# Kernel optimization log

Measured on AMD Instinct MI355X. Metric: run time of the kernel, lower is better.

Reference implementation:

```python
import jax, jax.numpy as jnp
import numpy as np

EPS = 1e-4


def setup_inputs() -> dict:
    key = jax.random.key(0)
    ks = jax.random.split(key, 16)
    N, D, H, K = 262144, 162, 256, 30
    s = 0.05  # weight init scale
    return {
        "Yh": jax.random.uniform(ks[0], (N, D), dtype=jnp.float32),
        "u": jax.random.uniform(ks[1], (1,), dtype=jnp.float32),
        "W1": jax.random.normal(ks[2], (D, H), dtype=jnp.float32) * s,
        "b1": jnp.zeros((H,), jnp.float32),
        "W2": jax.random.normal(ks[3], (H, H), dtype=jnp.float32) * s,
        "b2": jnp.zeros((H,), jnp.float32),
        "Wa": jax.random.normal(ks[4], (H, K), dtype=jnp.float32) * s,
        "ba": jnp.zeros((K,), jnp.float32),
        "Wb": jax.random.normal(ks[5], (H, K), dtype=jnp.float32) * s,
        "bb": jnp.zeros((K,), jnp.float32),
        "Wd1": jax.random.normal(ks[6], (K, H), dtype=jnp.float32) * s,
        "bd1": jnp.zeros((H,), jnp.float32),
        "Wd2": jax.random.normal(ks[7], (H, D), dtype=jnp.float32) * s,
        "bd2": jnp.zeros((D,), jnp.float32),
    }


def _stick_segments(v):
    # pi_k = v_k * prod_{j<k} (1 - v_j)  (vectorized exclusive cumprod,
    # replacing the original per-dim Python loop)
    cp = jnp.cumprod(1.0 - v, axis=1)  # [N, K]
    excl = jnp.concatenate([jnp.ones_like(v[:, :1]), cp[:, :-1]], axis=1)
    return v * excl


def reference(Yh, u, W1, b1, W2, b2, Wa, ba, Wb, bb, Wd1, bd1, Wd2, bd2):
    # encode_hsi: dense MLP -> positive Kumaraswamy params (softplus heads)
    h = jax.nn.relu(Yh @ W1 + b1)
    h = jax.nn.relu(h @ W2 + b2)
    alpha = jax.nn.softplus(h @ Wa + ba) + EPS  # param1_hsi [N, K]
    beta = jax.nn.softplus(h @ Wb + bb) + EPS   # param2_hsi [N, K]
    # Kumaraswamy reparametrization with a single shared uniform sample
    uu = u[0] * 0.98 + 0.01  # Uniform(0.01, 0.99) scalar
    v = (1.0 - uu ** (1.0 / beta)) ** (1.0 / alpha)  # [N, K]
    # set_v_K_to_one: force last stick proportion to 1
    v = jnp.concatenate([v[:, :-1], jnp.ones_like(v[:, :1])], axis=1)
    pi_h = _stick_segments(v)  # [N, K], rows sum to 1
    # decode: MLP -> sigmoid (positive outputs, recon.log() finite)
    d = jax.nn.relu(pi_h @ Wd1 + bd1)
    recon = jax.nn.sigmoid(d @ Wd2 + bd2)  # [N, D]
    return recon, alpha, beta, pi_h
```

## Files before the change

### kernel.cpp

```cpp
#include <hip/hip_runtime.h>
#include <hip/hip_bf16.h>

#define N_ROWS 262144
#define D_IN 162
#define K_DIM 30
#define ROWS 32

using bf16_t = __hip_bfloat16;
typedef __attribute__((ext_vector_type(8))) short bf16x8;
typedef __attribute__((ext_vector_type(4))) float f32x4;

__device__ __forceinline__ int swz_byte(int row, int col) {
  int b = (row << 9) + (col << 1);
  return b ^ ((row & 7) << 4);
}

__device__ __forceinline__ uint32_t bf16b(float x) {
  return (uint32_t)__builtin_bit_cast(unsigned short, __float2bfloat16(x));
}
__device__ __forceinline__ uint32_t pack2(float lo, float hi) {
  return bf16b(lo) | (bf16b(hi) << 16);
}
__device__ __forceinline__ float unpk_lo(uint32_t p) {
  return __bfloat162float(__builtin_bit_cast(__hip_bfloat16, (unsigned short)(p & 0xffff)));
}
__device__ __forceinline__ float unpk_hi(uint32_t p) {
  return __bfloat162float(__builtin_bit_cast(__hip_bfloat16, (unsigned short)(p >> 16)));
}
__device__ __forceinline__ float softplus_f(float x) {
  return (x > 15.f) ? x : log1pf(__expf(x));
}

__global__ void pack_b_kernel(const float* __restrict__ src, bf16_t* __restrict__ dst,
                              int K, int N, int Np, int KB) {
  int idx = blockIdx.x * 256 + threadIdx.x;
  int total = KB * Np * 32;
  if (idx >= total) return;
  int ks = idx & 31;
  int n  = (idx >> 5) % Np;
  int kb = idx / (32 * Np);
  int k  = kb * 32 + ks;
  float v = (k < K && n < N) ? src[k * N + n] : 0.f;
  dst[idx] = __float2bfloat16(v);
}

__global__ void pack_ab_kernel(const float* __restrict__ Wa, const float* __restrict__ Wb,
                               bf16_t* __restrict__ dst) {
  int idx = blockIdx.x * 256 + threadIdx.x;
  if (idx >= 8 * 64 * 32) return;
  int ks = idx & 31;
  int n  = (idx >> 5) & 63;
  int kb = idx >> 11;
  int k  = kb * 32 + ks;
  int j = n >> 1, s = n & 1;
  float v = (j < K_DIM) ? (s ? Wb[k * K_DIM + j] : Wa[k * K_DIM + j]) : 0.f;
  dst[idx] = __float2bfloat16(v);
}

template<int NP, int NMO>
__device__ __forceinline__ void wload(const bf16_t* __restrict__ Wp, int kb, int ocBase,
                                      int lr, int lg, bf16x8 (&out)[NMO]) {
#pragma unroll
  for (int mo = 0; mo < NMO; ++mo)
    out[mo] = *reinterpret_cast<const bf16x8*>(
        Wp + ((kb * NP + ocBase + 16 * mo + lr) << 5) + 8 * lg);
}

template<int KB, int NP, int NMO>
__device__ __forceinline__ void gemm_roll(const uint8_t* lds, int srcOff,
                                          const bf16_t* __restrict__ Wp, int ocBase,
                                          int lr, int lg, f32x4 (&acc)[NMO][2],
                                          bf16x8 (&wbuf)[2][NMO]) {
  int bE[2], bO[2];
#pragma unroll
  for (int nr = 0; nr < 2; ++nr) {
    bE[nr] = srcOff + swz_byte(16 * nr + lr, 8 * lg);
    bO[nr] = srcOff + swz_byte(16 * nr + lr, 32 + 8 * lg);
  }
#pragma unroll
  for (int kb = 0; kb < KB; ++kb) {
    bf16x8 cur[NMO];
#pragma unroll
    for (int mo = 0; mo < NMO; ++mo) cur[mo] = wbuf[kb & 1][mo];
    if (kb + 2 < KB)
      wload<NP, NMO>(Wp, kb + 2, ocBase, lr, lg, wbuf[kb & 1]);
    bf16x8 hf[2];
#pragma unroll
    for (int nr = 0; nr < 2; ++nr) {
      int base = (kb & 1) ? bO[nr] : bE[nr];
      hf[nr] = *reinterpret_cast<const bf16x8*>(lds + base + (kb >> 1) * 128);
    }
#pragma unroll
    for (int mo = 0; mo < NMO; ++mo)
#pragma unroll
      for (int nr = 0; nr < 2; ++nr)
        acc[mo][nr] = __builtin_amdgcn_mfma_f32_16x16x32_bf16(cur[mo], hf[nr], acc[mo][nr], 0, 0, 0);
  }
}

template<int NMO>
__device__ __forceinline__ void acc_bias_init(const float* __restrict__ bias, int ocBase,
                                              int lg, f32x4 (&acc)[NMO][2]) {
#pragma unroll
  for (int mo = 0; mo < NMO; ++mo) {
    float4 bv = *reinterpret_cast<const float4*>(bias + ocBase + 16 * mo + 4 * lg);
    f32x4 t = {bv.x, bv.y, bv.z, bv.w};
#pragma unroll
    for (int nr = 0; nr < 2; ++nr) acc[mo][nr] = t;
  }
}

template<int NMO>
__device__ __forceinline__ void epi_relu_store(uint8_t* lds, int dstOff, int ocBase,
                                               int lr, int lg, f32x4 (&acc)[NMO][2]) {
#pragma unroll
  for (int mo = 0; mo < NMO; ++mo)
#pragma unroll
    for (int nr = 0; nr < 2; ++nr) {
      int row = 16 * nr + lr;
      int col = ocBase + 16 * mo + 4 * lg;
      float x0 = fmaxf(acc[mo][nr][0], 0.f), x1 = fmaxf(acc[mo][nr][1], 0.f);
      float x2 = fmaxf(acc[mo][nr][2], 0.f), x3 = fmaxf(acc[mo][nr][3], 0.f);
      uint2 p; p.x = pack2(x0, x1); p.y = pack2(x2, x3);
      *reinterpret_cast<uint2*>(lds + dstOff + swz_byte(row, col)) = p;
    }
}

#define OFF_B  16384
#define OFF_PI (16384 + 8192)

__launch_bounds__(256, 4)
__global__ void usdn_fused(const float* __restrict__ Yh, const float* __restrict__ u,
                           const float* __restrict__ b1, const float* __restrict__ b2,
                           const float* __restrict__ ba, const float* __restrict__ bb,
                           const float* __restrict__ bd1, const float* __restrict__ bd2,
                           const bf16_t* __restrict__ Wp1, const bf16_t* __restrict__ Wp2,
                           const bf16_t* __restrict__ Wpab, const bf16_t* __restrict__ Wpd1,
                           const bf16_t* __restrict__ Wpd2,
                           float* __restrict__ outRecon, float* __restrict__ outAlpha,
                           float* __restrict__ outBeta, float* __restrict__ outPi) {
  __shared__ __align__(16) uint8_t lds[32768];

  const int tid = threadIdx.x;
  const int w  = tid >> 6;
  const int l  = tid & 63;
  const int lr = l & 15;
  const int lg = l >> 4;
  const int r0 = blockIdx.x * ROWS;

  const int srow = tid >> 3, sl8 = tid & 7;
  float2 sv[12];
  {
    const float2* src = reinterpret_cast<const float2*>(Yh + (size_t)(r0 + srow) * D_IN);
#pragma unroll
    for (int it = 0; it < 12; ++it) {
      int f2 = sl8 + it * 8;
      if (f2 < 81) sv[it] = src[f2];
    }
  }
  bf16x8 w1buf[2][4];
  wload<256, 4>(Wp1, 0, w * 64, lr, lg, w1buf[0]);
  wload<256, 4>(Wp1, 1, w * 64, lr, lg, w1buf[1]);
  {
#pragma unroll
    for (int it = 0; it < 12; ++it) {
      int f2 = sl8 + it * 8;
      uint32_t p = 0;
      if (f2 < 81) p = pack2(sv[it].x, sv[it].y);
      if (f2 < 96) *reinterpret_cast<uint32_t*>(lds + swz_byte(srow, f2 * 2)) = p;
    }
  }
  __syncthreads();

  bf16x8 w2buf[2][4];
  {
    f32x4 acc[4][2];
    acc_bias_init<4>(b1, w * 64, lg, acc);
    gemm_roll<6, 256, 4>(lds, 0, Wp1, w * 64, lr, lg, acc, w1buf);
    wload<256, 4>(Wp2, 0, w * 64, lr, lg, w2buf[0]);
    wload<256, 4>(Wp2, 1, w * 64, lr, lg, w2buf[1]);
    epi_relu_store<4>(lds, OFF_B, w * 64, lr, lg, acc);
  }
  __syncthreads();

  bf16x8 wh[8];
  {
    f32x4 acc[4][2];
    acc_bias_init<4>(b2, w * 64, lg, acc);
    gemm_roll<8, 256, 4>(lds, OFF_B, Wp2, w * 64, lr, lg, acc, w2buf);
#pragma unroll
    for (int kb = 0; kb < 8; ++kb)
      wh[kb] = *reinterpret_cast<const bf16x8*>(Wpab + ((kb * 64 + 16 * w + lr) << 5) + 8 * lg);
    epi_relu_store<4>(lds, 0, w * 64, lr, lg, acc);
  }
  __syncthreads();

  float regA0[2], regA1[2], regB0[2], regB1[2];
  const int j0 = 8 * w + 2 * lg;
  bf16x8 w4[4];
  bf16x8 w5buf[2][3];
  {
    bool jv = (j0 < K_DIM);
    float ba0 = jv ? ba[j0] : 0.f,     bb0 = jv ? bb[j0] : 0.f;
    float ba1 = jv ? ba[j0 + 1] : 0.f, bb1 = jv ? bb[j0 + 1] : 0.f;
    f32x4 acc[2];
    f32x4 binit = {ba0, bb0, ba1, bb1};
    acc[0] = binit; acc[1] = binit;
    int bE[2], bO[2];
#pragma unroll
    for (int nr = 0; nr < 2; ++nr) {
      bE[nr] = swz_byte(16 * nr + lr, 8 * lg);
      bO[nr] = swz_byte(16 * nr + lr, 32 + 8 * lg);
    }
#pragma unroll
    for (int kb = 0; kb < 8; ++kb) {
#pragma unroll
      for (int nr = 0; nr < 2; ++nr) {
        int base = (kb & 1) ? bO[nr] : bE[nr];
        bf16x8 hf = *reinterpret_cast<const bf16x8*>(lds + base + (kb >> 1) * 128);
        acc[nr] = __builtin_amdgcn_mfma_f32_16x16x32_bf16(wh[kb], hf, acc[nr], 0, 0, 0);
      }
    }
    wload<256, 4>(Wpd1, 0, w * 64, lr, lg, w4);
    wload<192, 3>(Wpd2, 0, 48 * w, lr, lg, w5buf[0]);
    wload<192, 3>(Wpd2, 1, 48 * w, lr, lg, w5buf[1]);

    float uu  = u[0] * 0.98f + 0.01f;
    float l2u = log2f(uu);
    float* vbuf = reinterpret_cast<float*>(lds + OFF_B);
#pragma unroll
    for (int nr = 0; nr < 2; ++nr) {
      int row = 16 * nr + lr;
      float a0  = softplus_f(acc[nr][0]) + 1e-4f;
      float b0v = softplus_f(acc[nr][1]) + 1e-4f;
      float a1  = softplus_f(acc[nr][2]) + 1e-4f;
      float b1v = softplus_f(acc[nr][3]) + 1e-4f;
      regA0[nr] = a0; regB0[nr] = b0v; regA1[nr] = a1; regB1[nr] = b1v;
      if (jv) {
        if (j0 < K_DIM - 1) {
          float t = exp2f(l2u / b0v);
          vbuf[row * 33 + j0] = exp2f(log2f(1.f - t) / a0);
        }
        if (j0 + 1 < K_DIM - 1) {
          float t = exp2f(l2u / b1v);
          vbuf[row * 33 + j0 + 1] = exp2f(log2f(1.f - t) / a1);
        }
      }
    }
  }
  __syncthreads();

  if (tid < ROWS) {
    const float* vbuf = reinterpret_cast<const float*>(lds + OFF_B);
    bf16_t* piT = reinterpret_cast<bf16_t*>(lds + OFF_PI);
    int row = tid;
    float ex = 1.f;
#pragma unroll
    for (int j = 0; j < K_DIM - 1; ++j) {
      float vj = vbuf[row * 33 + j];
      float pi = vj * ex;
      piT[row * 40 + j] = __float2bfloat16(pi);
      ex *= (1.f - vj);
    }
    piT[row * 40 + (K_DIM - 1)] = __float2bfloat16(ex);
    piT[row * 40 + 30] = __float2bfloat16(0.f);
    piT[row * 40 + 31] = __float2bfloat16(0.f);
  }
  __syncthreads();

  {
    f32x4 acc[4][2];
    acc_bias_init<4>(bd1, w * 64, lg, acc);
    bf16x8 pf[2];
#pragma unroll
    for (int nr = 0; nr < 2; ++nr)
      pf[nr] = *reinterpret_cast<const bf16x8*>(lds + OFF_PI + (16 * nr + lr) * 80 + 16 * lg);
#pragma unroll
    for (int mo = 0; mo < 4; ++mo)
#pragma unroll
      for (int nr = 0; nr < 2; ++nr)
        acc[mo][nr] = __builtin_amdgcn_mfma_f32_16x16x32_bf16(w4[mo], pf[nr], acc[mo][nr], 0, 0, 0);
    epi_relu_store<4>(lds, 0, w * 64, lr, lg, acc);
  }
  __syncthreads();

  {
    f32x4 acc[3][2];
#pragma unroll
    for (int mo = 0; mo < 3; ++mo) {
      int col0 = 48 * w + 16 * mo + 4 * lg;
      f32x4 t;
#pragma unroll
      for (int i = 0; i < 4; ++i) t[i] = (col0 + i < D_IN) ? bd2[col0 + i] : 0.f;
#pragma unroll
      for (int nr = 0; nr < 2; ++nr) acc[mo][nr] = t;
    }
    gemm_roll<8, 192, 3>(lds, 0, Wpd2, 48 * w, lr, lg, acc, w5buf);
#pragma unroll
    for (int mo = 0; mo < 3; ++mo) {
      int col0 = 48 * w + 16 * mo + 4 * lg;
#pragma unroll
      for (int nr = 0; nr < 2; ++nr) {
        int row = 16 * nr + lr;
        float s0 = 1.f / (1.f + __expf(-acc[mo][nr][0]));
        float s1 = 1.f / (1.f + __expf(-acc[mo][nr][1]));
        float s2 = 1.f / (1.f + __expf(-acc[mo][nr][2]));
        float s3 = 1.f / (1.f + __expf(-acc[mo][nr][3]));
        float* dst = outRecon + (size_t)(r0 + row) * D_IN + col0;
        if (col0 < D_IN)     *reinterpret_cast<float2*>(dst)     = make_float2(s0, s1);
        if (col0 + 2 < D_IN) *reinterpret_cast<float2*>(dst + 2) = make_float2(s2, s3);
      }
    }
  }

  if (j0 < K_DIM) {
#pragma unroll
    for (int nr = 0; nr < 2; ++nr) {
      int row = 16 * nr + lr;
      size_t base = (size_t)(r0 + row) * K_DIM + j0;
      *reinterpret_cast<float2*>(outAlpha + base) = make_float2(regA0[nr], regA1[nr]);
      *reinterpret_cast<float2*>(outBeta  + base) = make_float2(regB0[nr], regB1[nr]);
    }
  }
  {
    int row = tid >> 3, l8 = tid & 7;
#pragma unroll
    for (int half = 0; half < 2; ++half) {
      int f2 = l8 + half * 8;
      if (f2 < 15) {
        uint32_t pp = *reinterpret_cast<const uint32_t*>(lds + OFF_PI + row * 80 + f2 * 4);
        *reinterpret_cast<float2*>(outPi + (size_t)(r0 + row) * K_DIM + f2 * 2) =
            make_float2(unpk_lo(pp), unpk_hi(pp));
      }
    }
  }
}

extern "C" void kernel_launch(void* const* d_in, const int* in_sizes, int n_in,
                              void* d_out, int out_size, void* d_ws, size_t ws_size,
                              hipStream_t stream) {
  const float* Yh  = (const float*)d_in[0];
  const float* u   = (const float*)d_in[1];
  const float* W1  = (const float*)d_in[2];
  const float* b1  = (const float*)d_in[3];
  const float* W2  = (const float*)d_in[4];
  const float* b2  = (const float*)d_in[5];
  const float* Wa  = (const float*)d_in[6];
  const float* ba  = (const float*)d_in[7];
  const float* Wb  = (const float*)d_in[8];
  const float* bb  = (const float*)d_in[9];
  const float* Wd1 = (const float*)d_in[10];
  const float* bd1 = (const float*)d_in[11];
  const float* Wd2 = (const float*)d_in[12];
  const float* bd2 = (const float*)d_in[13];

  bf16_t* ws   = (bf16_t*)d_ws;
  bf16_t* Wp1  = ws;
  bf16_t* Wp2  = Wp1 + 49152;
  bf16_t* Wpab = Wp2 + 65536;
  bf16_t* Wpd1 = Wpab + 16384;
  bf16_t* Wpd2 = Wpd1 + 8192;

  float* outRecon = (float*)d_out;
  float* outAlpha = outRecon + (size_t)N_ROWS * D_IN;
  float* outBeta  = outAlpha + (size_t)N_ROWS * K_DIM;
  float* outPi    = outBeta  + (size_t)N_ROWS * K_DIM;

  pack_b_kernel<<<192, 256, 0, stream>>>(W1, Wp1, 162, 256, 256, 6);
  pack_b_kernel<<<256, 256, 0, stream>>>(W2, Wp2, 256, 256, 256, 8);
  pack_ab_kernel<<<64, 256, 0, stream>>>(Wa, Wb, Wpab);
  pack_b_kernel<<<32, 256, 0, stream>>>(Wd1, Wpd1, 30, 256, 256, 1);
  pack_b_kernel<<<192, 256, 0, stream>>>(Wd2, Wpd2, 256, 162, 192, 8);

  usdn_fused<<<N_ROWS / ROWS, 256, 0, stream>>>(Yh, u, b1, b2, ba, bb, bd1, bd2,
                                                Wp1, Wp2, Wpab, Wpd1, Wpd2,
                                                outRecon, outAlpha, outBeta, outPi);
}
```

Before: 269.9 us.

## Replace single-thread stick scan with redundant per-lane scan and fast intrinsics

Removes the serial 32-thread stick-breaking pass and its extra barrier: each lane now recomputes the full exclusive cumprod for its row and packs its own bf16 MFMA fragment directly, while warp 0 writes fp32 pi to LDS for output. This also stores pi_h in fp32 rather than a bf16 round-trip. Softplus, sigmoid and the Kumaraswamy pow chain switch to raw hardware exp2/log2/rcp intrinsics. Empty asm pins are added to keep the weight register prefetches in place. The cost is redundant scan work across all 256 threads and slightly lower accuracy from the approximate intrinsics.

```diff
diff --git a/kernel.cpp b/kernel.cpp
--- a/kernel.cpp
+++ b/kernel.cpp
@@ -21,14 +21,21 @@
 __device__ __forceinline__ uint32_t pack2(float lo, float hi) {
   return bf16b(lo) | (bf16b(hi) << 16);
 }
-__device__ __forceinline__ float unpk_lo(uint32_t p) {
-  return __bfloat162float(__builtin_bit_cast(__hip_bfloat16, (unsigned short)(p & 0xffff)));
-}
-__device__ __forceinline__ float unpk_hi(uint32_t p) {
-  return __bfloat162float(__builtin_bit_cast(__hip_bfloat16, (unsigned short)(p >> 16)));
-}
-__device__ __forceinline__ float softplus_f(float x) {
-  return (x > 15.f) ? x : log1pf(__expf(x));
+
+__device__ __forceinline__ float fexp2(float x) { return __builtin_amdgcn_exp2f(x); }
+__device__ __forceinline__ float flog2(float x) { return __builtin_amdgcn_logf(x); }
+__device__ __forceinline__ float frcp (float x) { return __builtin_amdgcn_rcpf(x); }
+
+__device__ __forceinline__ float sp_fast(float x) {
+  float e = fexp2(fabsf(x) * -1.44269504f);
+  return fmaxf(x, 0.f) + 0.69314718f * flog2(1.f + e);
+}
+__device__ __forceinline__ float sigmoid_fast(float x) {
+  return frcp(1.f + fexp2(x * -1.44269504f));
+}
+
+template<typename T> __device__ __forceinline__ void pin(T& x) {
+  asm volatile("" : "+v"(x));
 }
 
 __global__ void pack_b_kernel(const float* __restrict__ src, bf16_t* __restrict__ dst,
@@ -126,6 +133,32 @@
     }
 }
 
+template<int LG>
+__device__ __forceinline__ bf16x8 scan_frag(const float* __restrict__ vrow,
+                                            float* __restrict__ piOut) {
+  float ex = 1.f, hold = 0.f;
+  uint32_t pk0 = 0, pk1 = 0, pk2 = 0, pk3 = 0;
+#pragma unroll
+  for (int j = 0; j < 32; ++j) {
+    float pi;
+    if (j < K_DIM - 1)       { float vj = vrow[j]; pi = vj * ex; ex *= (1.f - vj); }
+    else if (j == K_DIM - 1)   pi = ex;
+    else                       pi = 0.f;
+    if (piOut != nullptr && j < K_DIM) piOut[j] = pi;
+    if (j >= 8 * LG && j < 8 * LG + 8) {
+      if (j & 1) {
+        uint32_t p = pack2(hold, pi);
+        switch ((j - 8 * LG) >> 1) {
+          case 0: pk0 = p; break; case 1: pk1 = p; break;
+          case 2: pk2 = p; break; default: pk3 = p;
+        }
+      } else hold = pi;
+    }
+  }
+  uint4 t = make_uint4(pk0, pk1, pk2, pk3);
+  return __builtin_bit_cast(bf16x8, t);
+}
+
 #define OFF_B  16384
 #define OFF_PI (16384 + 8192)
 
@@ -161,6 +194,8 @@
   bf16x8 w1buf[2][4];
   wload<256, 4>(Wp1, 0, w * 64, lr, lg, w1buf[0]);
   wload<256, 4>(Wp1, 1, w * 64, lr, lg, w1buf[1]);
+#pragma unroll
+  for (int mo = 0; mo < 4; ++mo) { pin(w1buf[0][mo]); pin(w1buf[1][mo]); }
   {
 #pragma unroll
     for (int it = 0; it < 12; ++it) {
@@ -179,6 +214,8 @@
     gemm_roll<6, 256, 4>(lds, 0, Wp1, w * 64, lr, lg, acc, w1buf);
     wload<256, 4>(Wp2, 0, w * 64, lr, lg, w2buf[0]);
     wload<256, 4>(Wp2, 1, w * 64, lr, lg, w2buf[1]);
+#pragma unroll
+    for (int mo = 0; mo < 4; ++mo) { pin(w2buf[0][mo]); pin(w2buf[1][mo]); }
     epi_relu_store<4>(lds, OFF_B, w * 64, lr, lg, acc);
   }
   __syncthreads();
@@ -189,8 +226,10 @@
     acc_bias_init<4>(b2, w * 64, lg, acc);
     gemm_roll<8, 256, 4>(lds, OFF_B, Wp2, w * 64, lr, lg, acc, w2buf);
 #pragma unroll
-    for (int kb = 0; kb < 8; ++kb)
+    for (int kb = 0; kb < 8; ++kb) {
       wh[kb] = *reinterpret_cast<const bf16x8*>(Wpab + ((kb * 64 + 16 * w + lr) << 5) + 8 * lg);
+      pin(wh[kb]);
+    }
     epi_relu_store<4>(lds, 0, w * 64, lr, lg, acc);
   }
   __syncthreads();
@@ -224,57 +263,52 @@
     wload<256, 4>(Wpd1, 0, w * 64, lr, lg, w4);
     wload<192, 3>(Wpd2, 0, 48 * w, lr, lg, w5buf[0]);
     wload<192, 3>(Wpd2, 1, 48 * w, lr, lg, w5buf[1]);
+#pragma unroll
+    for (int mo = 0; mo < 4; ++mo) pin(w4[mo]);
+#pragma unroll
+    for (int mo = 0; mo < 3; ++mo) { pin(w5buf[0][mo]); pin(w5buf[1][mo]); }
 
     float uu  = u[0] * 0.98f + 0.01f;
-    float l2u = log2f(uu);
+    float l2u = flog2(uu);
     float* vbuf = reinterpret_cast<float*>(lds + OFF_B);
 #pragma unroll
     for (int nr = 0; nr < 2; ++nr) {
       int row = 16 * nr + lr;
-      float a0  = softplus_f(acc[nr][0]) + 1e-4f;
-      float b0v = softplus_f(acc[nr][1]) + 1e-4f;
-      float a1  = softplus_f(acc[nr][2]) + 1e-4f;
-      float b1v = softplus_f(acc[nr][3]) + 1e-4f;
+      float a0  = sp_fast(acc[nr][0]) + 1e-4f;
+      float b0v = sp_fast(acc[nr][1]) + 1e-4f;
+      float a1  = sp_fast(acc[nr][2]) + 1e-4f;
+      float b1v = sp_fast(acc[nr][3]) + 1e-4f;
       regA0[nr] = a0; regB0[nr] = b0v; regA1[nr] = a1; regB1[nr] = b1v;
       if (jv) {
         if (j0 < K_DIM - 1) {
-          float t = exp2f(l2u / b0v);
-          vbuf[row * 33 + j0] = exp2f(log2f(1.f - t) / a0);
+          float t = fexp2(l2u * frcp(b0v));
+          vbuf[row * 36 + j0] = fexp2(flog2(1.f - t) * frcp(a0));
         }
         if (j0 + 1 < K_DIM - 1) {
-          float t = exp2f(l2u / b1v);
-          vbuf[row * 33 + j0 + 1] = exp2f(log2f(1.f - t) / a1);
+          float t = fexp2(l2u * frcp(b1v));
+          vbuf[row * 36 + j0 + 1] = fexp2(flog2(1.f - t) * frcp(a1));
         }
       }
     }
   }
   __syncthreads();
 
-  if (tid < ROWS) {
-    const float* vbuf = reinterpret_cast<const float*>(lds + OFF_B);
-    bf16_t* piT = reinterpret_cast<bf16_t*>(lds + OFF_PI);
-    int row = tid;
-    float ex = 1.f;
-#pragma unroll
-    for (int j = 0; j < K_DIM - 1; ++j) {
-      float vj = vbuf[row * 33 + j];
-      float pi = vj * ex;
-      piT[row * 40 + j] = __float2bfloat16(pi);
-      ex *= (1.f - vj);
-    }
-    piT[row * 40 + (K_DIM - 1)] = __float2bfloat16(ex);
-    piT[row * 40 + 30] = __float2bfloat16(0.f);
-    piT[row * 40 + 31] = __float2bfloat16(0.f);
-  }
-  __syncthreads();
-
   {
     f32x4 acc[4][2];
+    bf16x8 pf[2];
+    const float* vb  = reinterpret_cast<const float*>(lds + OFF_B);
+    float* piT = reinterpret_cast<float*>(lds + OFF_PI);
+#pragma unroll
+    for (int nr = 0; nr < 2; ++nr) {
+      int row = 16 * nr + lr;
+      const float* vrow = vb + row * 36;
+      float* po = (w == 0) ? (piT + row * 34) : nullptr;
+      if      (lg == 0) pf[nr] = scan_frag<0>(vrow, po);
+      else if (lg == 1) pf[nr] = scan_frag<1>(vrow, nullptr);
+      else if (lg == 2) pf[nr] = scan_frag<2>(vrow, nullptr);
+      else              pf[nr] = scan_frag<3>(vrow, nullptr);
+    }
     acc_bias_init<4>(bd1, w * 64, lg, acc);
-    bf16x8 pf[2];
-#pragma unroll
-    for (int nr = 0; nr < 2; ++nr)
-      pf[nr] = *reinterpret_cast<const bf16x8*>(lds + OFF_PI + (16 * nr + lr) * 80 + 16 * lg);
 #pragma unroll
     for (int mo = 0; mo < 4; ++mo)
 #pragma unroll
@@ -302,10 +336,10 @@
 #pragma unroll
       for (int nr = 0; nr < 2; ++nr) {
         int row = 16 * nr + lr;
-        float s0 = 1.f / (1.f + __expf(-acc[mo][nr][0]));
-        float s1 = 1.f / (1.f + __expf(-acc[mo][nr][1]));
-        float s2 = 1.f / (1.f + __expf(-acc[mo][nr][2]));
-        float s3 = 1.f / (1.f + __expf(-acc[mo][nr][3]));
+        float s0 = sigmoid_fast(acc[mo][nr][0]);
+        float s1 = sigmoid_fast(acc[mo][nr][1]);
+        float s2 = sigmoid_fast(acc[mo][nr][2]);
+        float s3 = sigmoid_fast(acc[mo][nr][3]);
         float* dst = outRecon + (size_t)(r0 + row) * D_IN + col0;
         if (col0 < D_IN)     *reinterpret_cast<float2*>(dst)     = make_float2(s0, s1);
         if (col0 + 2 < D_IN) *reinterpret_cast<float2*>(dst + 2) = make_float2(s2, s3);
@@ -323,14 +357,14 @@
     }
   }
   {
+    const float* piT = reinterpret_cast<const float*>(lds + OFF_PI);
     int row = tid >> 3, l8 = tid & 7;
 #pragma unroll
     for (int half = 0; half < 2; ++half) {
       int f2 = l8 + half * 8;
       if (f2 < 15) {
-        uint32_t pp = *reinterpret_cast<const uint32_t*>(lds + OFF_PI + row * 80 + f2 * 4);
-        *reinterpret_cast<float2*>(outPi + (size_t)(r0 + row) * K_DIM + f2 * 2) =
-            make_float2(unpk_lo(pp), unpk_hi(pp));
+        float2 pp = *reinterpret_cast<const float2*>(piT + row * 34 + f2 * 2);
+        *reinterpret_cast<float2*>(outPi + (size_t)(r0 + row) * K_DIM + f2 * 2) = pp;
       }
     }
   }
```

Measured after the change: 277.6 us. +2.9%, slower.
